# Kernel tuning notes

Measured on AMD Instinct MI355X. Metric: run time of the kernel, lower is better.

Reference implementation:

```python
import jax, jax.numpy as jnp
import numpy as np

B, N, T, L = 32, 716, 168, 64
SED, TED = 32, 4
TN_LAYERS, GCN_LAYERS = 2, 2
TCN_C = 16


def _gru_scan(xseq, Wih, Whh, bih, bhh):
    # torch nn.GRU (batch_first) math; xseq: (B,T,Din) -> (B,T,H)
    Bq = xseq.shape[0]
    H = Whh.shape[1]
    xw = xseq @ Wih.T + bih  # (B,T,3H)

    def step(h, xw_t):
        gh = h @ Whh.T + bhh
        xr, xz, xn = jnp.split(xw_t, 3, axis=-1)
        hr, hz, hn = jnp.split(gh, 3, axis=-1)
        r = jax.nn.sigmoid(xr + hr)
        z = jax.nn.sigmoid(xz + hz)
        n = jnp.tanh(xn + r * hn)
        h_new = (1.0 - z) * n + z * h
        return h_new, h_new

    h0 = jnp.zeros((Bq, H), xseq.dtype)
    _, hs = jax.lax.scan(step, h0, jnp.swapaxes(xw, 0, 1))
    return jnp.swapaxes(hs, 0, 1)


def setup_inputs() -> dict:
    key = jax.random.key(0)
    ks = jax.random.split(key, 20)
    r = lambda k, shp, s: jax.random.normal(k, shp, dtype=jnp.float32) * s
    z = lambda shp: jnp.zeros(shp, jnp.float32)
    din = T + SED
    gin = N + SED + TED
    inp = {
        'x': r(ks[0], (B, N, T), 1.0),
        'x_enc_mark': r(ks[1], (B, T, TED), 1.0),
        'se_emb': r(ks[2], (N, SED), 0.02),
        'se_W1': r(ks[3], (din, L), din ** -0.5), 'se_b1': z((L,)),
        'se_W2': r(ks[4], (L, L), L ** -0.5), 'se_b2': z((L,)),
        'te_emb': r(ks[5], (T, SED), 0.02),
        'te_Wih': r(ks[6], (3 * L, gin), gin ** -0.5),
        'te_Whh': r(ks[7], (3 * L, L), L ** -0.5),
        'te_bih': z((3 * L,)), 'te_bhh': z((3 * L,)),
        'gcn_W': r(ks[8], (TN_LAYERS, GCN_LAYERS, L, L), L ** -0.5),
        'gcn_b': z((TN_LAYERS, GCN_LAYERS, L)),
        'fr_W1': r(ks[9], (L, T), L ** -0.5), 'fr_b1': z((T,)),
        'fr_W2': r(ks[10], (T, T), T ** -0.5), 'fr_b2': z((T,)),
        'tr_Wih': r(ks[11], (3 * N, L), L ** -0.5),
        'tr_Whh': r(ks[12], (3 * N, N), N ** -0.5),
        'tr_bih': z((3 * N,)), 'tr_bhh': z((3 * N,)),
        'tcn_W0': r(ks[13], (TCN_C, 3, 1, 2), (3 * 2) ** -0.5), 'tcn_b0': z((TCN_C,)),
        'tcn_W1': r(ks[14], (TCN_C, TCN_C, 1, 2), (TCN_C * 2) ** -0.5), 'tcn_b1': z((TCN_C,)),
        'tcn_W2': r(ks[15], (TCN_C, TCN_C, 1, 2), (TCN_C * 2) ** -0.5), 'tcn_b2': z((TCN_C,)),
        'out_W': r(ks[16], (1, TCN_C, 1, 1), TCN_C ** -0.5), 'out_b': z((1,)),
    }
    return inp


def reference(x, x_enc_mark, se_emb, se_W1, se_b1, se_W2, se_b2,
              te_emb, te_Wih, te_Whh, te_bih, te_bhh,
              gcn_W, gcn_b, fr_W1, fr_b1, fr_W2, fr_b2,
              tr_Wih, tr_Whh, tr_bih, tr_bhh,
              tcn_W0, tcn_b0, tcn_W1, tcn_b1, tcn_W2, tcn_b2, out_W, out_b):
    Bq, Nq, Tq = x.shape
    elu = jax.nn.elu
    # ---- SpatialEncoder: (B,N,T) -> (B,N,L)
    se_in = jnp.concatenate([x, jnp.broadcast_to(se_emb, (Bq,) + se_emb.shape)], axis=2)
    Xs = elu(se_in @ se_W1 + se_b1) @ se_W2 + se_b2
    # ---- TemporalEncoder: GRU over (B,T,N+SED+TED) -> (B,T,L)
    te_in = jnp.concatenate([jnp.swapaxes(x, 1, 2), x_enc_mark,
                             jnp.broadcast_to(te_emb, (Bq,) + te_emb.shape)], axis=2)
    Xt = _gru_scan(te_in, te_Wih, te_Whh, te_bih, te_bhh)
    X = jnp.concatenate([Xs, Xt], axis=1)  # (B, N+T, L)
    # ---- TN modules: adaptive graph construction + message passing.
    # adj = tanh(relu(X X^T) + I). The torch code extracts nonzero edges per batch
    # and scatters messages over them; since zero weights contribute nothing,
    # edge-list message passing == dense weighted-adjacency matmul (vectorized here).
    eye = jnp.eye(Nq + Tq, dtype=x.dtype)
    for i in range(gcn_W.shape[0]):
        adj = jnp.tanh(jax.nn.relu(jnp.einsum('bnf,bmf->bnm', X, X)) + eye)
        h = X
        for j in range(gcn_W.shape[1]):
            h = elu(jnp.einsum('bnm,bmf->bnf', adj, h) @ gcn_W[i, j] + gcn_b[i, j])
        X = h
    Xs, Xt = X[:, :Nq, :], X[:, Nq:, :]
    # ---- rebuild heads
    n_out = elu(Xs @ fr_W1 + fr_b1) @ fr_W2 + fr_b2  # (B,N,T)
    t_out = _gru_scan(Xt, tr_Wih, tr_Whh, tr_bih, tr_bhh)  # (B,T,N)
    stacked = jnp.stack([n_out, jnp.swapaxes(t_out, 1, 2), x], axis=1)  # (B,3,N,T)
    # ---- TCN output layer: causal dilated convs along time, then 1x1 projection
    dn = ('NCHW', 'OIHW', 'NCHW')
    h = stacked
    for W, b, d in ((tcn_W0, tcn_b0, 1), (tcn_W1, tcn_b1, 2), (tcn_W2, tcn_b2, 4)):
        h = jax.lax.conv_general_dilated(h, W, (1, 1), ((0, 0), (d, 0)),
                                         rhs_dilation=(1, d), dimension_numbers=dn)
        h = elu(h + b[None, :, None, None])
    out = jax.lax.conv_general_dilated(h, out_W, (1, 1), 'VALID',
                                       dimension_numbers=dn) + out_b[None, :, None, None]
    return out[:, :, :, -1]  # (B, 1, N): one-step forecast per node
```

## Files before the change

kernel.cpp:

```cpp
#include <hip/hip_runtime.h>

#define B_   32
#define N_   716
#define T_   168
#define L_   64
#define NT_  884
#define NTP  896
#define TE3_ 192
#define TRH_ 716
#define TR3_ 2148
#define TR3P 2176
#define WSTR 744
#define HSTR 720
#define TRBLKS 90

typedef unsigned short u16;
typedef unsigned long long u64;
typedef __attribute__((ext_vector_type(8))) short short8;
typedef __attribute__((ext_vector_type(4))) float f32x4;

static __device__ __forceinline__ float eluf(float x){ return x > 0.f ? x : expm1f(x); }
static __device__ __forceinline__ float sigf(float x){ return 1.f/(1.f+expf(-x)); }
static __device__ __forceinline__ u16 f2bf(float f){
  unsigned u = __float_as_uint(f);
// ... 19 lines not shown
__global__ __launch_bounds__(256) void k_wihbf(const float* __restrict__ Wih, u16* __restrict__ WihB){
  int idx = blockIdx.x*256 + threadIdx.x;
  if (idx >= TR3P*L_) return;
  int r = idx >> 6;
  WihB[idx] = (r < TR3_) ? f2bf(Wih[idx]) : (u16)0;
}
__global__ __launch_bounds__(256) void k_wtb(const float* __restrict__ W,
                                             u16* __restrict__ WTh, u16* __restrict__ WTl){
  int l = blockIdx.x;
  for (int e = threadIdx.x; e < 4096; e += 256){
    int g = e >> 6, f = e & 63;
    float v = W[(size_t)l*4096 + f*64 + g];
    u16 hi = f2bf(v);
    WTh[(size_t)l*4096 + e] = hi;
    WTl[(size_t)l*4096 + e] = f2bf(v - bf2f(hi));
  }
}
__global__ __launch_bounds__(256) void k_sew(const float* __restrict__ W1, const float* __restrict__ W2,
    u16* __restrict__ w1h, u16* __restrict__ w1l, u16* __restrict__ w2h, u16* __restrict__ w2l){
  int tid = threadIdx.x;
  for (int e = tid; e < 64*224; e += 256){
    int g = e / 224, k = e % 224;
    float v = (k < 200) ? W1[k*64 + g] : 0.f;
    u16 hi = f2bf(v); w1h[e] = hi; w1l[e] = f2bf(v - bf2f(hi));
  }
  for (int e = tid; e < 4096; e += 256){
    int g = e >> 6, f = e & 63;
    float v = W2[f*64 + g];
    u16 hi = f2bf(v); w2h[e] = hi; w2l[e] = f2bf(v - bf2f(hi));
  }
}
__global__ __launch_bounds__(256) void k_frw(const float* __restrict__ W1, const float* __restrict__ W2,
    u16* __restrict__ w1h, u16* __restrict__ w1l, u16* __restrict__ w2h, u16* __restrict__ w2l){
  int tid = threadIdx.x;
  for (int e = tid; e < 176*64; e += 256){
    int n = e >> 6, k = e & 63;
    float v = (n < 168) ? W1[k*168 + n] : 0.f;
    u16 hi = f2bf(v); w1h[e] = hi; w1l[e] = f2bf(v - bf2f(hi));
  }
  for (int e = tid; e < 16*192; e += 256){
    int c = e / 192, k = e % 192;
    float v = (c < 8 && k < 168) ? W2[k*168 + 160 + c] : 0.f;
    u16 hi = f2bf(v); w2h[e] = hi; w2l[e] = f2bf(v - bf2f(hi));
  }
}
__global__ __launch_bounds__(256) void k_wte(const float* __restrict__ W, u16* __restrict__ wh, u16* __restrict__ wl){
  int idx = blockIdx.x*256 + threadIdx.x;
  if (idx >= 192*768) return;
  int g = idx / 768, k = idx % 768;
  float v = (k < 752) ? W[(size_t)g*752 + k] : 0.f;
  u16 hi = f2bf(v); wh[idx] = hi; wl[idx] = f2bf(v - bf2f(hi));
}

__global__ __launch_bounds__(256) void k_seinB(const float* __restrict__ x, const float* __restrict__ se_emb,
                                               u16* __restrict__ seh, u16* __restrict__ sel){
  int idx = blockIdx.x*256 + threadIdx.x;
  if (idx >= 22912*224) return;
  int k = idx % 224; int m = idx / 224;
  int b = m / N_, n = m - b*N_;
  float v = 0.f;
  if (k < 168) v = x[((size_t)b*N_ + n)*T_ + k];
  else if (k < 200) v = se_emb[n*32 + (k - 168)];
  u16 hi = f2bf(v);
  seh[idx] = hi; sel[idx] = f2bf(v - bf2f(hi));
}

__global__ __launch_bounds__(256) void k_sem(const u16* __restrict__ seh, const u16* __restrict__ sel,
    const u16* __restrict__ w1h, const u16* __restrict__ w1l,
    const u16* __restrict__ w2h, const u16* __restrict__ w2l,
    const float* __restrict__ b1, const float* __restrict__ b2, float* __restrict__ X){
  __shared__ u16 Tlh[64*72], Tll[64*72];
  int m0 = blockIdx.x*64;
  int tid = threadIdx.x, wv = tid >> 6, lane = tid & 63;
  const u16* Ah = seh + (size_t)(m0 + 16*wv + (lane & 15))*224 + (lane >> 4)*8;
  const u16* Al = sel + (size_t)(m0 + 16*wv + (lane & 15))*224 + (lane >> 4)*8;
  const u16* Bh = w1h + (lane & 15)*224 + (lane >> 4)*8;
  const u16* Bl = w1l + (lane & 15)*224 + (lane >> 4)*8;
  f32x4 hh[4], hl[4], lh[4];
  #pragma unroll
  for (int q = 0; q < 4; ++q){ hh[q]=(f32x4){0,0,0,0}; hl[q]=(f32x4){0,0,0,0}; lh[q]=(f32x4){0,0,0,0}; }
  #pragma unroll
  for (int kt = 0; kt < 7; ++kt){
    short8 ah = *(const short8*)(Ah + kt*32);
    short8 al = *(const short8*)(Al + kt*32);
    #pragma unroll
    for (int q = 0; q < 4; ++q){
      short8 bh = *(const short8*)(Bh + q*16*224 + kt*32);
      short8 bl = *(const short8*)(Bl + q*16*224 + kt*32);
      hh[q] = bmfma(ah, bh, hh[q]);
      hl[q] = bmfma(ah, bl, hl[q]);
      lh[q] = bmfma(al, bh, lh[q]);
    }
  }
  int mrow = 16*wv + (lane >> 4)*4;
  #pragma unroll
  for (int q = 0; q < 4; ++q){
    int g = q*16 + (lane & 15);
    float bv = b1[g];
    #pragma unroll
    for (int r = 0; r < 4; ++r){
      float v = eluf(hh[q][r] + hl[q][r] + lh[q][r] + bv);
      u16 hi = f2bf(v);
      Tlh[(mrow + r)*72 + g] = hi;
      Tll[(mrow + r)*72 + g] = f2bf(v - bf2f(hi));
    }
  }
  __syncthreads();
  const u16* A2h = Tlh + (16*wv + (lane & 15))*72 + (lane >> 4)*8;
  const u16* A2l = Tll + (16*wv + (lane & 15))*72 + (lane >> 4)*8;
  const u16* B2h = w2h + (lane & 15)*64 + (lane >> 4)*8;
  const u16* B2l = w2l + (lane & 15)*64 + (lane >> 4)*8;
  f32x4 ohh[4], ohl[4], olh[4];
  #pragma unroll
  for (int q = 0; q < 4; ++q){ ohh[q]=(f32x4){0,0,0,0}; ohl[q]=(f32x4){0,0,0,0}; olh[q]=(f32x4){0,0,0,0}; }
  #pragma unroll
  for (int kt = 0; kt < 2; ++kt){
    short8 a2h = *(const short8*)(A2h + kt*32);
    short8 a2l = *(const short8*)(A2l + kt*32);
    #pragma unroll
    for (int q = 0; q < 4; ++q){
      short8 b2h = *(const short8*)(B2h + q*16*64 + kt*32);
      short8 b2l = *(const short8*)(B2l + q*16*64 + kt*32);
      ohh[q] = bmfma(a2h, b2h, ohh[q]);
      ohl[q] = bmfma(a2h, b2l, ohl[q]);
      olh[q] = bmfma(a2l, b2h, olh[q]);
    }
  }
  #pragma unroll
// ... 39 lines not shown
  else if (c < 36) v = te_emb[t*32 + (c - 4)];
  u16 hi = f2bf(v);
  size_t o = (size_t)row*768 + 716 + c;
  th_[o] = hi; tl_[o] = f2bf(v - bf2f(hi));
}

__global__ __launch_bounds__(256) void k_texw(const u16* __restrict__ teh, const u16* __restrict__ tel,
    const u16* __restrict__ wh, const u16* __restrict__ wl,
    const float* __restrict__ bih, float* __restrict__ xwte){
  int m0 = blockIdx.x*64, n0 = blockIdx.y*64;
  int tid = threadIdx.x, wv = tid >> 6, lane = tid & 63;
  const u16* Ah = teh + (size_t)(m0 + 16*wv + (lane & 15))*768 + (lane >> 4)*8;
  const u16* Al = tel + (size_t)(m0 + 16*wv + (lane & 15))*768 + (lane >> 4)*8;
  const u16* Bh = wh + (size_t)(n0 + (lane & 15))*768 + (lane >> 4)*8;
  const u16* Bl = wl + (size_t)(n0 + (lane & 15))*768 + (lane >> 4)*8;
  f32x4 hh[4], hl[4], lh[4];
  #pragma unroll
  for (int q = 0; q < 4; ++q){ hh[q]=(f32x4){0,0,0,0}; hl[q]=(f32x4){0,0,0,0}; lh[q]=(f32x4){0,0,0,0}; }
  #pragma unroll 4
  for (int kt = 0; kt < 24; ++kt){
    short8 ah = *(const short8*)(Ah + kt*32);
    short8 al = *(const short8*)(Al + kt*32);
    #pragma unroll
    for (int q = 0; q < 4; ++q){
      short8 bh = *(const short8*)(Bh + q*16*768 + kt*32);
      short8 bl = *(const short8*)(Bl + q*16*768 + kt*32);
      hh[q] = bmfma(ah, bh, hh[q]);
      hl[q] = bmfma(ah, bl, hl[q]);
      lh[q] = bmfma(al, bh, lh[q]);
    }
  }
  int mb = m0 + 16*wv + (lane >> 4)*4;
  #pragma unroll
  for (int q = 0; q < 4; ++q){
    int g = n0 + q*16 + (lane & 15);
    float bv = bih[g];
    #pragma unroll
    for (int r = 0; r < 4; ++r)
      xwte[(size_t)(mb + r)*TE3_ + g] = hh[q][r] + hl[q][r] + lh[q][r] + bv;
  }
}

__global__ __launch_bounds__(192) void k_te_scan(const float* __restrict__ xw, const float* __restrict__ Whh,
                 const float* __restrict__ bhh, float* __restrict__ X){
  int b = blockIdx.x; int tid = threadIdx.x;
  __shared__ float Wsh[TE3_*65];
  __shared__ float hs[64];
  __shared__ float gh[TE3_];
  for (int l = tid; l < TE3_*64; l += 192){ int j = l >> 6, f = l & 63; Wsh[j*65+f] = Whh[l]; }
  if (tid < 64) hs[tid] = 0.f;
  __syncthreads();
  for (int t = 0; t < T_; ++t){
    const float* xr = xw + ((size_t)b*T_ + t)*TE3_;
    float g = bhh[tid];
    #pragma unroll 8
    for (int f = 0; f < 64; ++f) g = fmaf(hs[f], Wsh[tid*65+f], g);
    gh[tid] = g;
    __syncthreads();
    if (tid < 64){
      float r = sigf(xr[tid] + gh[tid]);
      float z = sigf(xr[64+tid] + gh[64+tid]);
      float n = tanhf(xr[128+tid] + r*gh[128+tid]);
      float hn = (1.f - z)*n + z*hs[tid];
      hs[tid] = hn;
      X[((size_t)b*NT_ + N_ + t)*L_ + tid] = hn;
    }
    __syncthreads();
  }
}

__global__ __launch_bounds__(256) void k_xbf(const float* __restrict__ X,
                 u16* __restrict__ Xbh, u16* __restrict__ Xbl,
                 u16* __restrict__ XTh, u16* __restrict__ XTl){
  __shared__ u16 th[32][33], tl[32][33];
  int b = blockIdx.z, i0 = blockIdx.x*32, f0 = blockIdx.y*32;
  int tx = threadIdx.x & 31, ty = threadIdx.x >> 5;
  for (int rr = ty; rr < 32; rr += 8){
    int i = i0 + rr, f = f0 + tx;
    float v = (i < NT_) ? X[((size_t)b*NT_ + i)*L_ + f] : 0.f;
    u16 hi = f2bf(v);
    u16 lo = f2bf(v - bf2f(hi));
    th[rr][tx] = hi; tl[rr][tx] = lo;
    Xbh[((size_t)b*NTP + i)*L_ + f] = hi;
    Xbl[((size_t)b*NTP + i)*L_ + f] = lo;
  }
  __syncthreads();
  for (int rr = ty; rr < 32; rr += 8){
    XTh[((size_t)b*L_ + f0 + rr)*NTP + i0 + tx] = th[tx][rr];
    XTl[((size_t)b*L_ + f0 + rr)*NTP + i0 + tx] = tl[tx][rr];
  }
}

__global__ __launch_bounds__(256) void k_adjb(const u16* __restrict__ Xbh, const u16* __restrict__ Xbl,
                                              u16* __restrict__ adjh, u16* __restrict__ adjl){
  int b = blockIdx.z, i0 = blockIdx.x*64, j0 = blockIdx.y*64;
  int tid = threadIdx.x, wv = tid >> 6, lane = tid & 63;
  const u16* Ah = Xbh + ((size_t)b*NTP + i0 + 16*wv + (lane & 15))*L_ + (lane >> 4)*8;
  const u16* Al = Xbl + ((size_t)b*NTP + i0 + 16*wv + (lane & 15))*L_ + (lane >> 4)*8;
  const u16* Bh = Xbh + ((size_t)b*NTP + j0 + (lane & 15))*L_ + (lane >> 4)*8;
  const u16* Bl = Xbl + ((size_t)b*NTP + j0 + (lane & 15))*L_ + (lane >> 4)*8;
  f32x4 chh[4], chl[4], clh[4];
  #pragma unroll
  for (int q = 0; q < 4; ++q){ chh[q] = (f32x4){0,0,0,0}; chl[q] = (f32x4){0,0,0,0}; clh[q] = (f32x4){0,0,0,0}; }
  #pragma unroll
  for (int kt = 0; kt < 2; ++kt){
    short8 ah = *(const short8*)(Ah + kt*32);
    short8 al = *(const short8*)(Al + kt*32);
    #pragma unroll
    for (int q = 0; q < 4; ++q){
      short8 bh = *(const short8*)(Bh + q*16*L_ + kt*32);
      short8 bl = *(const short8*)(Bl + q*16*L_ + kt*32);
      chh[q] = bmfma(ah, bh, chh[q]);
      chl[q] = bmfma(ah, bl, chl[q]);
      clh[q] = bmfma(al, bh, clh[q]);
    }
  }
  int ib = i0 + 16*wv + (lane >> 4)*4;
  int jb = j0 + (lane & 15);
  #pragma unroll
  for (int q = 0; q < 4; ++q){
    int j = jb + q*16;
    #pragma unroll
    for (int r = 0; r < 4; ++r){
      int i = ib + r;
      size_t idx = ((size_t)b*NTP + i)*NTP + j;
      if (i < NT_ && j < NT_){
        float v = tanhf(fmaxf(chh[q][r] + chl[q][r] + clh[q][r], 0.f) + (i == j ? 1.f : 0.f));
        u16 hi = f2bf(v);
        adjh[idx] = hi;
        adjl[idx] = f2bf(v - bf2f(hi));
      } else {
        adjh[idx] = 0; adjl[idx] = 0;
      }
    }
  }
}

__global__ __launch_bounds__(256) void k_gcnm(const u16* __restrict__ adjh, const u16* __restrict__ adjl,
                 const u16* __restrict__ hTh, const u16* __restrict__ hTl,
                 const u16* __restrict__ WTh, const u16* __restrict__ WTl,
                 const float* __restrict__ bias,
                 float* __restrict__ Y, u16* __restrict__ YTh, u16* __restrict__ YTl){
  __shared__ u16 Tlh[64*72], Tll[64*72];
  int b = blockIdx.y, i0 = blockIdx.x*64;
  int tid = threadIdx.x, wv = tid >> 6, lane = tid & 63;
  const u16* Ah = adjh + ((size_t)b*NTP + i0 + 16*wv + (lane & 15))*NTP + (lane >> 4)*8;
  const u16* Al = adjl + ((size_t)b*NTP + i0 + 16*wv + (lane & 15))*NTP + (lane >> 4)*8;
  const u16* Bh = hTh + ((size_t)b*L_ + (lane & 15))*NTP + (lane >> 4)*8;
  const u16* Bl = hTl + ((size_t)b*L_ + (lane & 15))*NTP + (lane >> 4)*8;
  f32x4 thh[4], thl[4], tlh[4];
  #pragma unroll
  for (int q = 0; q < 4; ++q){ thh[q] = (f32x4){0,0,0,0}; thl[q] = (f32x4){0,0,0,0}; tlh[q] = (f32x4){0,0,0,0}; }
  #pragma unroll 2
  for (int kt = 0; kt < 28; ++kt){
    short8 ah = *(const short8*)(Ah + kt*32);
    short8 al = *(const short8*)(Al + kt*32);
    #pragma unroll
    for (int q = 0; q < 4; ++q){
      short8 bh = *(const short8*)(Bh + q*16*NTP + kt*32);
      short8 bl = *(const short8*)(Bl + q*16*NTP + kt*32);
      thh[q] = bmfma(ah, bh, thh[q]);
      thl[q] = bmfma(ah, bl, thl[q]);
      tlh[q] = bmfma(al, bh, tlh[q]);
    }
  }
  {
    int mrow = 16*wv + (lane >> 4)*4;
    #pragma unroll
    for (int q = 0; q < 4; ++q)
      #pragma unroll
      for (int r = 0; r < 4; ++r){
        float v = thh[q][r] + thl[q][r] + tlh[q][r];
        u16 hi = f2bf(v);
        Tlh[(mrow + r)*72 + q*16 + (lane & 15)] = hi;
        Tll[(mrow + r)*72 + q*16 + (lane & 15)] = f2bf(v - bf2f(hi));
      }
  }
  __syncthreads();
  const u16* A2h = Tlh + (16*wv + (lane & 15))*72 + (lane >> 4)*8;
  const u16* A2l = Tll + (16*wv + (lane & 15))*72 + (lane >> 4)*8;
  const u16* B2h = WTh + (lane & 15)*L_ + (lane >> 4)*8;
  const u16* B2l = WTl + (lane & 15)*L_ + (lane >> 4)*8;
  f32x4 ohh[4], ohl[4], olh[4];
  #pragma unroll
  for (int q = 0; q < 4; ++q){ ohh[q] = (f32x4){0,0,0,0}; ohl[q] = (f32x4){0,0,0,0}; olh[q] = (f32x4){0,0,0,0}; }
  #pragma unroll
  for (int kt = 0; kt < 2; ++kt){
    short8 a2h = *(const short8*)(A2h + kt*32);
    short8 a2l = *(const short8*)(A2l + kt*32);
    #pragma unroll
    for (int q = 0; q < 4; ++q){
      short8 b2h = *(const short8*)(B2h + q*16*L_ + kt*32);
      short8 b2l = *(const short8*)(B2l + q*16*L_ + kt*32);
      ohh[q] = bmfma(a2h, b2h, ohh[q]);
      ohl[q] = bmfma(a2h, b2l, ohl[q]);
      olh[q] = bmfma(a2l, b2h, olh[q]);
    }
  }
  __syncthreads();
  {
    int mrow = 16*wv + (lane >> 4)*4;
    #pragma unroll
    for (int q = 0; q < 4; ++q){
      int g = q*16 + (lane & 15);
      float bv = bias[g];
      #pragma unroll
      for (int r = 0; r < 4; ++r){
        int i = i0 + mrow + r;
        float v = eluf(ohh[q][r] + ohl[q][r] + olh[q][r] + bv);
        if (i < NT_ && Y) Y[((size_t)b*NT_ + i)*L_ + g] = v;
        u16 hi = 0, lo = 0;
        if (i < NT_){ hi = f2bf(v); lo = f2bf(v - bf2f(hi)); }
        Tlh[g*72 + mrow + r] = hi;
        Tll[g*72 + mrow + r] = lo;
      }
    }
  }
  __syncthreads();
  {
    int g = tid >> 2, c = tid & 3;
    uint4* dh = (uint4*)(YTh + ((size_t)b*L_ + g)*NTP + i0 + c*16);
    uint4* dl = (uint4*)(YTl + ((size_t)b*L_ + g)*NTP + i0 + c*16);
    const uint4* sh = (const uint4*)(Tlh + g*72 + c*16);
    const uint4* sl = (const uint4*)(Tll + g*72 + c*16);
    dh[0] = sh[0]; dh[1] = sh[1];
    dl[0] = sl[0]; dl[1] = sl[1];
  }
}

__global__ __launch_bounds__(256) void k_frm(const u16* __restrict__ Xbh, const u16* __restrict__ Xbl,
    const u16* __restrict__ w1h, const u16* __restrict__ w1l,
    const u16* __restrict__ w2h, const u16* __restrict__ w2l,
    const float* __restrict__ b1, const float* __restrict__ b2, float* __restrict__ nout8){
  __shared__ u16 T1h[64*192], T1l[64*192];
  __shared__ u16 B2hl[16*192], B2ll[16*192];
  int m0 = blockIdx.x*64;
  int tid = threadIdx.x, wv = tid >> 6, lane = tid & 63;
  for (int o = tid; o < 768; o += 256){
    ((u64*)B2hl)[o] = ((const u64*)w2h)[o];
    ((u64*)B2ll)[o] = ((const u64*)w2l)[o];
  }
  for (int o = tid; o < 1024; o += 256){
    int rr = o >> 4, cc = o & 15;
    T1h[rr*192 + 176 + cc] = 0; T1l[rr*192 + 176 + cc] = 0;
  }
  int ar = m0 + 16*wv + (lane & 15);
  int ab = ar / N_, an = ar - ab*N_;
  const u16* Ah = Xbh + ((size_t)ab*NTP + an)*L_ + (lane >> 4)*8;
  const u16* Al = Xbl + ((size_t)ab*NTP + an)*L_ + (lane >> 4)*8;
  int mrow = 16*wv + (lane >> 4)*4;
  for (int tile = 0; tile < 11; ++tile){
    const u16* Bh = w1h + (tile*16 + (lane & 15))*64 + (lane >> 4)*8;
    const u16* Bl = w1l + (tile*16 + (lane & 15))*64 + (lane >> 4)*8;
    f32x4 shh={0,0,0,0}, shl={0,0,0,0}, slh={0,0,0,0};
    #pragma unroll
    for (int kt = 0; kt < 2; ++kt){
      short8 ah = *(const short8*)(Ah + kt*32);
      short8 al = *(const short8*)(Al + kt*32);
      short8 bh = *(const short8*)(Bh + kt*32);
      short8 bl = *(const short8*)(Bl + kt*32);
      shh = bmfma(ah, bh, shh);
      shl = bmfma(ah, bl, shl);
      slh = bmfma(al, bh, slh);
    }
    int col = tile*16 + (lane & 15);
    float bb = (col < 168) ? b1[col] : 0.f;
    #pragma unroll
    for (int r = 0; r < 4; ++r){
// ... 31 lines not shown
}

__global__ __launch_bounds__(256) void k_xtbufb(const float* __restrict__ X, u16* __restrict__ XtB){
  int idx = blockIdx.x*256 + threadIdx.x;
  if (idx >= T_*B_*L_) return;
  int f = idx & 63; int tb = idx >> 6; int bb = tb & 31; int t = tb >> 5;
  XtB[idx] = f2bf(X[((size_t)bb*NT_ + N_ + t)*L_ + f]);
}

__global__ __launch_bounds__(256) void k_xwm(const u16* __restrict__ XtB, const u16* __restrict__ WihB,
                                             const float* __restrict__ bih, float* __restrict__ xw){
  int m0 = blockIdx.x*64, n0 = blockIdx.y*64;
  int tid = threadIdx.x, wv = tid >> 6, lane = tid & 63;
  const u16* Ab = XtB + (size_t)(m0 + 16*wv + (lane & 15))*L_ + (lane >> 4)*8;
  const u16* Bb = WihB + (size_t)(n0 + (lane & 15))*L_ + (lane >> 4)*8;
  f32x4 c0={0,0,0,0}, c1={0,0,0,0}, c2={0,0,0,0}, c3={0,0,0,0};
  #pragma unroll
  for (int kt = 0; kt < 2; ++kt){
    short8 a = *(const short8*)(Ab + kt*32);
    c0 = bmfma(a, *(const short8*)(Bb + kt*32), c0);
    c1 = bmfma(a, *(const short8*)(Bb + 16*L_ + kt*32), c1);
    c2 = bmfma(a, *(const short8*)(Bb + 32*L_ + kt*32), c2);
    c3 = bmfma(a, *(const short8*)(Bb + 48*L_ + kt*32), c3);
  }
  int mb = m0 + 16*wv + (lane >> 4)*4;
  int nb = n0 + (lane & 15);
  f32x4 cc[4] = {c0, c1, c2, c3};
  #pragma unroll
  for (int q = 0; q < 4; ++q){
    int n = nb + q*16;
    if (n >= TR3_) continue;
    float bv = bih[n];
    #pragma unroll
    for (int r = 0; r < 4; ++r)
      xw[(size_t)(mb + r)*TR3_ + n] = cc[q][r] + bv;
  }
}

__global__ __launch_bounds__(192) void k_tr_scan(
    const u16* __restrict__ WhhB,
    const float* __restrict__ bhh,
    const float* __restrict__ xw,
    u16* __restrict__ hb0, u16* __restrict__ hb1,
    float* __restrict__ tout8,
    int* __restrict__ flags){
  __shared__ u16 w_lds[48*WSTR];
  __shared__ u16 h_lds[16*WSTR];
  __shared__ float g_lds[2*256];
  __shared__ float xw_lds[2][16*48];
  const int tid = threadIdx.x;
  const int wv = tid >> 6, lane = tid & 63;
  const int cb = blockIdx.x >> 1, hhalf = blockIdx.x & 1;
  const int k0 = cb*16, b0 = hhalf*16;

  {
    int row = tid / 12, c = tid % 12;
    int g = c >> 2, koff = (c & 3)*4;
    *(f32x4*)(&xw_lds[0][row*48 + g*16 + koff]) =
      *(const f32x4*)(xw + (size_t)(b0 + row)*TR3_ + g*TRH_ + k0 + koff);
  }
  for (int o = tid; o < 16*24; o += 192){
    int n = o / 24, c = o - n*24;
    h_lds[n*WSTR + 720 + c] = 0;
  }
  for (int r = 0; r < 48; ++r){
    int g = r >> 4, m = r & 15, k = k0 + m;
    bool kv = (k < TRH_);
    const uint2* src = (const uint2*)(WhhB + (size_t)(g*TRH_ + (kv ? k : 0))*TRH_);
    uint2* dst = (uint2*)(w_lds + r*WSTR);
    uint2 zz; zz.x = 0; zz.y = 0;
    for (int o = tid; o < 186; o += 192)
      dst[o] = (kv && o < 179) ? src[o] : zz;
  }
  const u16* arow = w_lds + (size_t)(wv*16 + (lane & 15))*WSTR + (lane >> 4)*8;
  const u16* brow = h_lds + (size_t)(lane & 15)*WSTR + (lane >> 4)*8;

  const int mb = (lane >> 4)*4;
  const int kx = k0 + mb;
  const bool kval = (kx < TRH_);
  const int bx = b0 + (lane & 15);
  f32x4 hp = {0.f, 0.f, 0.f, 0.f};
  f32x4 br4 = {0,0,0,0}, bz4 = {0,0,0,0}, bn4 = {0,0,0,0};
  if (wv == 0){
    int kc = kval ? kx : 0;
    br4 = *(const f32x4*)(bhh + kc);
    bz4 = *(const f32x4*)(bhh + TRH_ + kc);
    bn4 = *(const f32x4*)(bhh + 2*TRH_ + kc);
  }
  const int sn = tid / 12, sj = tid % 12;
  u16* const ldst = h_lds + sn*WSTR + sj*8;
  __syncthreads();

  for (int t = 0; t < T_; ++t){
    const u16* hcur = (t & 1) ? hb1 : hb0;
    u16* hnxt = (t & 1) ? hb0 : hb1;
    if (tid < 45){
      const int* fp = flags + (tid*2 + hhalf)*16;
      while (__hip_atomic_load(fp, __ATOMIC_RELAXED, __HIP_MEMORY_SCOPE_AGENT) < t){}
    }
    __syncthreads();
    {
      const u64* srow = (const u64*)(hcur + (size_t)(b0 + sn)*HSTR) + sj;
      u64 v0  = __hip_atomic_load(srow +   0, __ATOMIC_RELAXED, __HIP_MEMORY_SCOPE_AGENT);
      u64 v1  = __hip_atomic_load(srow +  12, __ATOMIC_RELAXED, __HIP_MEMORY_SCOPE_AGENT);
      u64 v2  = __hip_atomic_load(srow +  24, __ATOMIC_RELAXED, __HIP_MEMORY_SCOPE_AGENT);
      u64 v3  = __hip_atomic_load(srow +  36, __ATOMIC_RELAXED, __HIP_MEMORY_SCOPE_AGENT);
      u64 v4  = __hip_atomic_load(srow +  48, __ATOMIC_RELAXED, __HIP_MEMORY_SCOPE_AGENT);
      u64 v5  = __hip_atomic_load(srow +  60, __ATOMIC_RELAXED, __HIP_MEMORY_SCOPE_AGENT);
      u64 v6  = __hip_atomic_load(srow +  72, __ATOMIC_RELAXED, __HIP_MEMORY_SCOPE_AGENT);
      u64 v7  = __hip_atomic_load(srow +  84, __ATOMIC_RELAXED, __HIP_MEMORY_SCOPE_AGENT);
      u64 v8  = __hip_atomic_load(srow +  96, __ATOMIC_RELAXED, __HIP_MEMORY_SCOPE_AGENT);
      u64 v9  = __hip_atomic_load(srow + 108, __ATOMIC_RELAXED, __HIP_MEMORY_SCOPE_AGENT);
      u64 v10 = __hip_atomic_load(srow + 120, __ATOMIC_RELAXED, __HIP_MEMORY_SCOPE_AGENT);
      u64 v11 = __hip_atomic_load(srow + 132, __ATOMIC_RELAXED, __HIP_MEMORY_SCOPE_AGENT);
      u64 v12 = __hip_atomic_load(srow + 144, __ATOMIC_RELAXED, __HIP_MEMORY_SCOPE_AGENT);
      u64 v13 = __hip_atomic_load(srow + 156, __ATOMIC_RELAXED, __HIP_MEMORY_SCOPE_AGENT);
      u64 v14 = __hip_atomic_load(srow + 168, __ATOMIC_RELAXED, __HIP_MEMORY_SCOPE_AGENT);
      u64* d = (u64*)(h_lds + sn*WSTR) + sj;
      d[0]      = v0;   d[12]     = v1;   d[24]     = v2;   d[36]     = v3;
      d[48]     = v4;   d[60]     = v5;   d[72]     = v6;   d[84]     = v7;
      d[96]     = v8;   d[108]    = v9;   d[120]    = v10;  d[132]    = v11;
      d[144]    = v12;  d[156]    = v13;  d[168]    = v14;
    }
    __syncthreads();
    f32x4 a0={0,0,0,0}, a1={0,0,0,0}, a2={0,0,0,0}, a3={0,0,0,0};
    for (int kt = 0; kt < 20; kt += 4){
      a0 = bmfma(*(const short8*)(arow + kt*32),     *(const short8*)(brow + kt*32),     a0);
      a1 = bmfma(*(const short8*)(arow + (kt+1)*32), *(const short8*)(brow + (kt+1)*32), a1);
      a2 = bmfma(*(const short8*)(arow + (kt+2)*32), *(const short8*)(brow + (kt+2)*32), a2);
      a3 = bmfma(*(const short8*)(arow + (kt+3)*32), *(const short8*)(brow + (kt+3)*32), a3);
    }
    a0 = bmfma(*(const short8*)(arow + 20*32), *(const short8*)(brow + 20*32), a0);
    a1 = bmfma(*(const short8*)(arow + 21*32), *(const short8*)(brow + 21*32), a1);
    a2 = bmfma(*(const short8*)(arow + 22*32), *(const short8*)(brow + 22*32), a2);
    f32x4 acc = (a0 + a1) + (a2 + a3);
    if (wv){
      #pragma unroll
      for (int r = 0; r < 4; ++r) g_lds[(wv-1)*256 + lane*4 + r] = acc[r];
    }
    __syncthreads();
    if (wv == 0 && kval){
      const float* xb = &xw_lds[t & 1][(lane & 15)*48];
      float hnew[4];
      #pragma unroll
      for (int r = 0; r < 4; ++r){
        float rg = sigf(xb[mb + r] + acc[r] + br4[r]);
        float zg = sigf(xb[16 + mb + r] + g_lds[lane*4 + r] + bz4[r]);
        float ng = tanhf(xb[32 + mb + r] + rg*(g_lds[256 + lane*4 + r] + bn4[r]));
        hnew[r] = (1.f - zg)*ng + zg*hp[r];
        hp[r] = hnew[r];
      }
      u64 pk = (u64)((unsigned)f2bf(hnew[0]) | ((unsigned)f2bf(hnew[1]) << 16))
             | ((u64)((unsigned)f2bf(hnew[2]) | ((unsigned)f2bf(hnew[3]) << 16)) << 32);
      __hip_atomic_store((u64*)(hnxt + (size_t)bx*HSTR + kx), pk,
                         __ATOMIC_RELAXED, __HIP_MEMORY_SCOPE_AGENT);
      if (t >= 160){
        #pragma unroll
        for (int r = 0; r < 4; ++r)
          tout8[(size_t)(bx*TRH_ + kx + r)*8 + (t - 160)] = hnew[r];
      }
    }
    if (wv == 0){
      asm volatile("s_waitcnt vmcnt(0)" ::: "memory");
      if (lane == 0)
        __hip_atomic_store(flags + blockIdx.x*16, t + 1,
                           __ATOMIC_RELAXED, __HIP_MEMORY_SCOPE_AGENT);
    }
    if (t + 1 < T_){
      int row = tid / 12, c = tid % 12;
      int g = c >> 2, koff = (c & 3)*4;
      *(f32x4*)(&xw_lds[(t + 1) & 1][row*48 + g*16 + koff]) =
        *(const f32x4*)(xw + (size_t)((t+1)*32 + b0 + row)*TR3_ + g*TRH_ + k0 + koff);
    }
  }
  (void)ldst;
}

__global__ __launch_bounds__(256) void k_tcn(const float* __restrict__ nout8, const float* __restrict__ tout8,
                 const float* __restrict__ x,
                 const float* __restrict__ W0, const float* __restrict__ b0,
                 const float* __restrict__ W1, const float* __restrict__ b1,
                 const float* __restrict__ W2, const float* __restrict__ b2,
                 const float* __restrict__ oW, const float* __restrict__ ob,
                 float* __restrict__ out){
  __shared__ float w0s[96], b0s[16], w1s[512], b1s[16], w2s[512], b2s[16], ows[16], obs;
  int tid = threadIdx.x;
  for (int l = tid; l < 96; l += 256) w0s[l] = W0[l];
  for (int l = tid; l < 512; l += 256){ w1s[l] = W1[l]; w2s[l] = W2[l]; }
  if (tid < 16){ b0s[tid]=b0[tid]; b1s[tid]=b1[tid]; b2s[tid]=b2[tid]; ows[tid]=oW[tid]; }
  if (tid == 0) obs = ob[0];
  __syncthreads();
  int idx = blockIdx.x*256 + tid;
  if (idx >= B_*N_) return;
  int b = idx / N_, n = idx % N_;
  float s0[8], s1[8], s2[8];
  #pragma unroll
  for (int i = 0; i < 8; ++i){
    s0[i] = nout8[(size_t)idx*8 + i];
    s1[i] = tout8[(size_t)idx*8 + i];
    s2[i] = x[((size_t)b*N_ + n)*T_ + 160 + i];
  }
  float h1[16][4];
  #pragma unroll
  for (int c = 0; c < 16; ++c)
    #pragma unroll
    for (int q = 0; q < 4; ++q){
      int tt = 2*q + 1;
      float v = b0s[c]
        + w0s[c*6+0]*s0[tt-1] + w0s[c*6+1]*s0[tt]
        + w0s[c*6+2]*s1[tt-1] + w0s[c*6+3]*s1[tt]
        + w0s[c*6+4]*s2[tt-1] + w0s[c*6+5]*s2[tt];
      h1[c][q] = eluf(v);
    }
  float h2[16][2];
  #pragma unroll
  for (int c = 0; c < 16; ++c){
    float v3 = b1s[c], v7 = b1s[c];
    #pragma unroll
    for (int i2 = 0; i2 < 16; ++i2){
      v3 += w1s[c*32+i2*2]*h1[i2][0] + w1s[c*32+i2*2+1]*h1[i2][1];
      v7 += w1s[c*32+i2*2]*h1[i2][2] + w1s[c*32+i2*2+1]*h1[i2][3];
    }
    h2[c][0] = eluf(v3); h2[c][1] = eluf(v7);
  }
  float o = obs;
  #pragma unroll
  for (int c = 0; c < 16; ++c){
    float v = b2s[c];
// ... 27 lines not shown
  const float* fr_W2   = (const float*)d_in[16];
  const float* fr_b2   = (const float*)d_in[17];
  const float* tr_Wih  = (const float*)d_in[18];
  const float* tr_Whh  = (const float*)d_in[19];
  const float* tr_bih  = (const float*)d_in[20];
  const float* tr_bhh  = (const float*)d_in[21];
  const float* tcn_W0  = (const float*)d_in[22];
  const float* tcn_b0  = (const float*)d_in[23];
  const float* tcn_W1  = (const float*)d_in[24];
  const float* tcn_b1  = (const float*)d_in[25];
  const float* tcn_W2  = (const float*)d_in[26];
  const float* tcn_b2  = (const float*)d_in[27];
  const float* out_W   = (const float*)d_in[28];
  const float* out_b   = (const float*)d_in[29];
  float* out = (float*)d_out;
  (void)in_sizes; (void)n_in; (void)out_size; (void)ws_size;

  char* ws = (char*)d_ws;
  size_t off = 0;
  auto alloc = [&](size_t bytes)->void*{
    void* p = (void*)(ws + off); off += (bytes + 255) & ~(size_t)255; return p; };
  float* X       = (float*)alloc((size_t)B_*NT_*L_*4);
  u16*   adjh    = (u16*)  alloc((size_t)B_*NTP*NTP*2);
  u16*   adjl    = (u16*)  alloc((size_t)B_*NTP*NTP*2);
  u16*   XtB     = (u16*)  alloc((size_t)T_*B_*L_*2);
  u16*   WihB    = (u16*)  alloc((size_t)TR3P*L_*2);
  u16*   WhhB    = (u16*)  alloc((size_t)TR3_*TRH_*2);
  u16*   Xbh     = (u16*)  alloc((size_t)B_*NTP*L_*2);
  u16*   Xbl     = (u16*)  alloc((size_t)B_*NTP*L_*2);
  u16*   hTah    = (u16*)  alloc((size_t)B_*L_*NTP*2);
  u16*   hTal    = (u16*)  alloc((size_t)B_*L_*NTP*2);
  u16*   hTbh    = (u16*)  alloc((size_t)B_*L_*NTP*2);
  u16*   hTbl    = (u16*)  alloc((size_t)B_*L_*NTP*2);
  u16*   WTh     = (u16*)  alloc((size_t)4*4096*2);
  u16*   WTl     = (u16*)  alloc((size_t)4*4096*2);
  u16*   w1seh   = (u16*)  alloc((size_t)64*224*2);
  u16*   w1sel   = (u16*)  alloc((size_t)64*224*2);
  u16*   w2seh   = (u16*)  alloc((size_t)4096*2);
  u16*   w2sel   = (u16*)  alloc((size_t)4096*2);
  u16*   w1frh   = (u16*)  alloc((size_t)176*64*2);
  u16*   w1frl   = (u16*)  alloc((size_t)176*64*2);
  u16*   w2frh   = (u16*)  alloc((size_t)16*192*2);
  u16*   w2frl   = (u16*)  alloc((size_t)16*192*2);
  u16*   wteh    = (u16*)  alloc((size_t)192*768*2);
  u16*   wtel    = (u16*)  alloc((size_t)192*768*2);
  u16*   hb0     = (u16*)  alloc((size_t)B_*HSTR*2);
  u16*   hb1     = (u16*)  alloc((size_t)B_*HSTR*2);
  int*   flags   = (int*)  alloc(8192);
  float* nout8   = (float*)alloc((size_t)B_*N_*8*4);
  float* tout8   = (float*)alloc((size_t)B_*N_*8*4);
  u16*   teinh   = (u16*)adjh;
  u16*   teinl   = (u16*)((char*)adjh +  8257536);
  float* te_xw   = (float*)((char*)adjh + 16515072);
  u16*   seh     = (u16*)((char*)adjh + 20643840);
  u16*   sel     = (u16*)((char*)adjh + 30908416);
  float* xw      = (float*)adjl;

  hipMemsetAsync(hb0, 0, (size_t)B_*HSTR*2*2 + 8192, stream);

  k_whhbf<<<(TR3_*TRH_/4 + 255)/256, 256, 0, stream>>>(tr_Whh, WhhB, TR3_*TRH_/4);
  k_wihbf<<<(TR3P*L_ + 255)/256, 256, 0, stream>>>(tr_Wih, WihB);
  k_wtb<<<4, 256, 0, stream>>>(gcn_W, WTh, WTl);
  k_sew<<<1, 256, 0, stream>>>(se_W1, se_W2, w1seh, w1sel, w2seh, w2sel);
  k_frw<<<1, 256, 0, stream>>>(fr_W1, fr_W2, w1frh, w1frl, w2frh, w2frl);
  k_wte<<<(192*768 + 255)/256, 256, 0, stream>>>(te_Wih, wteh, wtel);
  k_seinB<<<(22912*224 + 255)/256, 256, 0, stream>>>(x, se_emb, seh, sel);
  k_sem<<<358, 256, 0, stream>>>(seh, sel, w1seh, w1sel, w2seh, w2sel, se_b1, se_b2, X);
  k_teinx_b<<<dim3(23,6,B_), 256, 0, stream>>>(x, teinh, teinl);
  k_teinr_b<<<(B_*T_*52 + 255)/256, 256, 0, stream>>>(mark, te_emb, teinh, teinl);
  k_texw<<<dim3(84,3), 256, 0, stream>>>(teinh, teinl, wteh, wtel, te_bih, te_xw);
  k_te_scan<<<B_, 192, 0, stream>>>(te_xw, te_Whh, te_bhh, X);
  for (int i = 0; i < 2; ++i){
    k_xbf<<<dim3(28,2,B_),256,0,stream>>>(X, Xbh, Xbl, hTah, hTal);
    k_adjb<<<dim3(14,14,B_),256,0,stream>>>(Xbh, Xbl, adjh, adjl);
    k_gcnm<<<dim3(14,B_),256,0,stream>>>(adjh, adjl, hTah, hTal,
        WTh + (i*2+0)*4096, WTl + (i*2+0)*4096, gcn_b + (i*2+0)*64, nullptr, hTbh, hTbl);
    k_gcnm<<<dim3(14,B_),256,0,stream>>>(adjh, adjl, hTbh, hTbl,
        WTh + (i*2+1)*4096, WTl + (i*2+1)*4096, gcn_b + (i*2+1)*64, X, hTah, hTal);
  }
  k_xbf<<<dim3(28,2,B_),256,0,stream>>>(X, Xbh, Xbl, hTah, hTal);
  k_frm<<<358, 256, 0, stream>>>(Xbh, Xbl, w1frh, w1frl, w2frh, w2frl, fr_b1, fr_b2, nout8);
  k_xtbufb<<<(T_*B_*L_+255)/256,256,0,stream>>>(X, XtB);
  k_xwm<<<dim3(84,34),256,0,stream>>>(XtB, WihB, tr_bih, xw);
  k_tr_scan<<<TRBLKS,192,0,stream>>>(WhhB, tr_bhh, xw, hb0, hb1, tout8, flags);
  k_tcn<<<(B_*N_+255)/256,256,0,stream>>>(nout8, tout8, x,
      tcn_W0, tcn_b0, tcn_W1, tcn_b1, tcn_W2, tcn_b2, out_W, out_b, out);
}
```

Measured before the change: 1.447 ms.

## Fuse adjacency build into GCN matmul, fuse SE input conversion, prefetch scan inputs

Replaces the separate adjacency kernel plus the GCN kernel with one fused kernel. Each 64-row block recomputes 64x64 adjacency tiles from X in shared memory and consumes them right away, so the full bf16 hi/lo adjacency matrices are never written to or read from global memory. The adjacency is now recomputed in both GCN layers, so the X·X^T work is done twice per iteration. Separately, the SE input split/convert is moved into the SE matmul kernel via shared memory, the TE scan dot product gets four independent accumulators, the final xbf call skips its unused transpose, and the TR scan issues its next-step xw load before the MFMA loop.

```diff
diff --git a/kernel.cpp b/kernel.cpp
--- a/kernel.cpp
+++ b/kernel.cpp
@@ -95,28 +95,26 @@
   u16 hi = f2bf(v); wh[idx] = hi; wl[idx] = f2bf(v - bf2f(hi));
 }
 
-__global__ __launch_bounds__(256) void k_seinB(const float* __restrict__ x, const float* __restrict__ se_emb,
-                                               u16* __restrict__ seh, u16* __restrict__ sel){
-  int idx = blockIdx.x*256 + threadIdx.x;
-  if (idx >= 22912*224) return;
-  int k = idx % 224; int m = idx / 224;
-  int b = m / N_, n = m - b*N_;
-  float v = 0.f;
-  if (k < 168) v = x[((size_t)b*N_ + n)*T_ + k];
-  else if (k < 200) v = se_emb[n*32 + (k - 168)];
-  u16 hi = f2bf(v);
-  seh[idx] = hi; sel[idx] = f2bf(v - bf2f(hi));
-}
-
-__global__ __launch_bounds__(256) void k_sem(const u16* __restrict__ seh, const u16* __restrict__ sel,
+__global__ __launch_bounds__(256) void k_sem(const float* __restrict__ x, const float* __restrict__ se_emb,
     const u16* __restrict__ w1h, const u16* __restrict__ w1l,
     const u16* __restrict__ w2h, const u16* __restrict__ w2l,
     const float* __restrict__ b1, const float* __restrict__ b2, float* __restrict__ X){
+  __shared__ u16 Sh[64*232], Sl[64*232];
   __shared__ u16 Tlh[64*72], Tll[64*72];
   int m0 = blockIdx.x*64;
   int tid = threadIdx.x, wv = tid >> 6, lane = tid & 63;
-  const u16* Ah = seh + (size_t)(m0 + 16*wv + (lane & 15))*224 + (lane >> 4)*8;
-  const u16* Al = sel + (size_t)(m0 + 16*wv + (lane & 15))*224 + (lane >> 4)*8;
+  for (int o = tid; o < 64*224; o += 256){
+    int r = o / 224, k = o - (o/224)*224;
+    int m = m0 + r; int b = m / N_, n = m - b*N_;
+    float v = 0.f;
+    if (k < 168) v = x[((size_t)b*N_ + n)*T_ + k];
+    else if (k < 200) v = se_emb[n*32 + (k - 168)];
+    u16 hi = f2bf(v);
+    Sh[r*232 + k] = hi; Sl[r*232 + k] = f2bf(v - bf2f(hi));
+  }
+  __syncthreads();
+  const u16* Ah = Sh + (16*wv + (lane & 15))*232 + (lane >> 4)*8;
+  const u16* Al = Sl + (16*wv + (lane & 15))*232 + (lane >> 4)*8;
   const u16* Bh = w1h + (lane & 15)*224 + (lane >> 4)*8;
   const u16* Bl = w1l + (lane & 15)*224 + (lane >> 4)*8;
   f32x4 hh[4], hl[4], lh[4];
@@ -262,10 +260,15 @@
   __syncthreads();
   for (int t = 0; t < T_; ++t){
     const float* xr = xw + ((size_t)b*T_ + t)*TE3_;
-    float g = bhh[tid];
-    #pragma unroll 8
-    for (int f = 0; f < 64; ++f) g = fmaf(hs[f], Wsh[tid*65+f], g);
-    gh[tid] = g;
+    float g0 = bhh[tid], g1 = 0.f, g2 = 0.f, g3 = 0.f;
+    #pragma unroll
+    for (int f = 0; f < 64; f += 4){
+      g0 = fmaf(hs[f],   Wsh[tid*65+f],   g0);
+      g1 = fmaf(hs[f+1], Wsh[tid*65+f+1], g1);
+      g2 = fmaf(hs[f+2], Wsh[tid*65+f+2], g2);
+      g3 = fmaf(hs[f+3], Wsh[tid*65+f+3], g3);
+    }
+    gh[tid] = (g0 + g1) + (g2 + g3);
     __syncthreads();
     if (tid < 64){
       float r = sigf(xr[tid] + gh[tid]);
@@ -294,6 +297,7 @@
     Xbh[((size_t)b*NTP + i)*L_ + f] = hi;
     Xbl[((size_t)b*NTP + i)*L_ + f] = lo;
   }
+  if (!XTh) return;
   __syncthreads();
   for (int rr = ty; rr < 32; rr += 8){
     XTh[((size_t)b*L_ + f0 + rr)*NTP + i0 + tx] = th[tx][rr];
@@ -301,91 +305,92 @@
   }
 }
 
-__global__ __launch_bounds__(256) void k_adjb(const u16* __restrict__ Xbh, const u16* __restrict__ Xbl,
-                                              u16* __restrict__ adjh, u16* __restrict__ adjl){
-  int b = blockIdx.z, i0 = blockIdx.x*64, j0 = blockIdx.y*64;
-  int tid = threadIdx.x, wv = tid >> 6, lane = tid & 63;
-  const u16* Ah = Xbh + ((size_t)b*NTP + i0 + 16*wv + (lane & 15))*L_ + (lane >> 4)*8;
-  const u16* Al = Xbl + ((size_t)b*NTP + i0 + 16*wv + (lane & 15))*L_ + (lane >> 4)*8;
-  const u16* Bh = Xbh + ((size_t)b*NTP + j0 + (lane & 15))*L_ + (lane >> 4)*8;
-  const u16* Bl = Xbl + ((size_t)b*NTP + j0 + (lane & 15))*L_ + (lane >> 4)*8;
-  f32x4 chh[4], chl[4], clh[4];
-  #pragma unroll
-  for (int q = 0; q < 4; ++q){ chh[q] = (f32x4){0,0,0,0}; chl[q] = (f32x4){0,0,0,0}; clh[q] = (f32x4){0,0,0,0}; }
-  #pragma unroll
-  for (int kt = 0; kt < 2; ++kt){
-    short8 ah = *(const short8*)(Ah + kt*32);
-    short8 al = *(const short8*)(Al + kt*32);
-    #pragma unroll
-    for (int q = 0; q < 4; ++q){
-      short8 bh = *(const short8*)(Bh + q*16*L_ + kt*32);
-      short8 bl = *(const short8*)(Bl + q*16*L_ + kt*32);
-      chh[q] = bmfma(ah, bh, chh[q]);
-      chl[q] = bmfma(ah, bl, chl[q]);
-      clh[q] = bmfma(al, bh, clh[q]);
-    }
-  }
-  int ib = i0 + 16*wv + (lane >> 4)*4;
-  int jb = j0 + (lane & 15);
-  #pragma unroll
-  for (int q = 0; q < 4; ++q){
-    int j = jb + q*16;
-    #pragma unroll
-    for (int r = 0; r < 4; ++r){
-      int i = ib + r;
-      size_t idx = ((size_t)b*NTP + i)*NTP + j;
-      if (i < NT_ && j < NT_){
-        float v = tanhf(fmaxf(chh[q][r] + chl[q][r] + clh[q][r], 0.f) + (i == j ? 1.f : 0.f));
-        u16 hi = f2bf(v);
-        adjh[idx] = hi;
-        adjl[idx] = f2bf(v - bf2f(hi));
-      } else {
-        adjh[idx] = 0; adjl[idx] = 0;
-      }
-    }
-  }
-}
-
-__global__ __launch_bounds__(256) void k_gcnm(const u16* __restrict__ adjh, const u16* __restrict__ adjl,
-                 const u16* __restrict__ hTh, const u16* __restrict__ hTl,
-                 const u16* __restrict__ WTh, const u16* __restrict__ WTl,
-                 const float* __restrict__ bias,
-                 float* __restrict__ Y, u16* __restrict__ YTh, u16* __restrict__ YTl){
+__global__ __launch_bounds__(256) void k_gcnf(
+    const u16* __restrict__ Xbh, const u16* __restrict__ Xbl,
+    const u16* __restrict__ hTh, const u16* __restrict__ hTl,
+    const u16* __restrict__ WTh, const u16* __restrict__ WTl,
+    const float* __restrict__ bias,
+    float* __restrict__ Y, u16* __restrict__ YTh, u16* __restrict__ YTl){
+  __shared__ u16 AJh[64*72], AJl[64*72];
   __shared__ u16 Tlh[64*72], Tll[64*72];
   int b = blockIdx.y, i0 = blockIdx.x*64;
   int tid = threadIdx.x, wv = tid >> 6, lane = tid & 63;
-  const u16* Ah = adjh + ((size_t)b*NTP + i0 + 16*wv + (lane & 15))*NTP + (lane >> 4)*8;
-  const u16* Al = adjl + ((size_t)b*NTP + i0 + 16*wv + (lane & 15))*NTP + (lane >> 4)*8;
-  const u16* Bh = hTh + ((size_t)b*L_ + (lane & 15))*NTP + (lane >> 4)*8;
-  const u16* Bl = hTl + ((size_t)b*L_ + (lane & 15))*NTP + (lane >> 4)*8;
+  const u16* XAh = Xbh + ((size_t)b*NTP + i0 + 16*wv + (lane & 15))*L_ + (lane >> 4)*8;
+  const u16* XAl = Xbl + ((size_t)b*NTP + i0 + 16*wv + (lane & 15))*L_ + (lane >> 4)*8;
+  const int ib = i0 + 16*wv + (lane >> 4)*4;
+  const int mrow = 16*wv + (lane >> 4)*4;
   f32x4 thh[4], thl[4], tlh[4];
   #pragma unroll
   for (int q = 0; q < 4; ++q){ thh[q] = (f32x4){0,0,0,0}; thl[q] = (f32x4){0,0,0,0}; tlh[q] = (f32x4){0,0,0,0}; }
-  #pragma unroll 2
-  for (int kt = 0; kt < 28; ++kt){
-    short8 ah = *(const short8*)(Ah + kt*32);
-    short8 al = *(const short8*)(Al + kt*32);
-    #pragma unroll
-    for (int q = 0; q < 4; ++q){
-      short8 bh = *(const short8*)(Bh + q*16*NTP + kt*32);
-      short8 bl = *(const short8*)(Bl + q*16*NTP + kt*32);
-      thh[q] = bmfma(ah, bh, thh[q]);
-      thl[q] = bmfma(ah, bl, thl[q]);
-      tlh[q] = bmfma(al, bh, tlh[q]);
-    }
-  }
-  {
-    int mrow = 16*wv + (lane >> 4)*4;
-    #pragma unroll
-    for (int q = 0; q < 4; ++q)
+  for (int jt = 0; jt < 14; ++jt){
+    int j0 = jt*64;
+    {
+      const u16* XBh = Xbh + ((size_t)b*NTP + j0 + (lane & 15))*L_ + (lane >> 4)*8;
+      const u16* XBl = Xbl + ((size_t)b*NTP + j0 + (lane & 15))*L_ + (lane >> 4)*8;
+      f32x4 chh[4], chl[4], clh[4];
       #pragma unroll
-      for (int r = 0; r < 4; ++r){
-        float v = thh[q][r] + thl[q][r] + tlh[q][r];
-        u16 hi = f2bf(v);
-        Tlh[(mrow + r)*72 + q*16 + (lane & 15)] = hi;
-        Tll[(mrow + r)*72 + q*16 + (lane & 15)] = f2bf(v - bf2f(hi));
+      for (int q = 0; q < 4; ++q){ chh[q] = (f32x4){0,0,0,0}; chl[q] = (f32x4){0,0,0,0}; clh[q] = (f32x4){0,0,0,0}; }
+      #pragma unroll
+      for (int kt = 0; kt < 2; ++kt){
+        short8 ah = *(const short8*)(XAh + kt*32);
+        short8 al = *(const short8*)(XAl + kt*32);
+        #pragma unroll
+        for (int q = 0; q < 4; ++q){
+          short8 bh = *(const short8*)(XBh + q*16*L_ + kt*32);
+          short8 bl = *(const short8*)(XBl + q*16*L_ + kt*32);
+          chh[q] = bmfma(ah, bh, chh[q]);
+          chl[q] = bmfma(ah, bl, chl[q]);
+          clh[q] = bmfma(al, bh, clh[q]);
+        }
       }
-  }
+      int jb = j0 + (lane & 15);
+      #pragma unroll
+      for (int q = 0; q < 4; ++q){
+        int j = jb + q*16;
+        #pragma unroll
+        for (int r = 0; r < 4; ++r){
+          int i = ib + r;
+          u16 hi = 0, lo = 0;
+          if (i < NT_ && j < NT_){
+            float v = tanhf(fmaxf(chh[q][r] + chl[q][r] + clh[q][r], 0.f) + (i == j ? 1.f : 0.f));
+            hi = f2bf(v); lo = f2bf(v - bf2f(hi));
+          }
+          AJh[(mrow + r)*72 + q*16 + (lane & 15)] = hi;
+          AJl[(mrow + r)*72 + q*16 + (lane & 15)] = lo;
+        }
+      }
+    }
+    __syncthreads();
+    {
+      const u16* A1h = AJh + (16*wv + (lane & 15))*72 + (lane >> 4)*8;
+      const u16* A1l = AJl + (16*wv + (lane & 15))*72 + (lane >> 4)*8;
+      const u16* B1h = hTh + ((size_t)b*L_ + (lane & 15))*NTP + j0 + (lane >> 4)*8;
+      const u16* B1l = hTl + ((size_t)b*L_ + (lane & 15))*NTP + j0 + (lane >> 4)*8;
+      #pragma unroll
+      for (int kt = 0; kt < 2; ++kt){
+        short8 ah = *(const short8*)(A1h + kt*32);
+        short8 al = *(const short8*)(A1l + kt*32);
+        #pragma unroll
+        for (int q = 0; q < 4; ++q){
+          short8 bh = *(const short8*)(B1h + q*16*NTP + kt*32);
+          short8 bl = *(const short8*)(B1l + q*16*NTP + kt*32);
+          thh[q] = bmfma(ah, bh, thh[q]);
+          thl[q] = bmfma(ah, bl, thl[q]);
+          tlh[q] = bmfma(al, bh, tlh[q]);
+        }
+      }
+    }
+    __syncthreads();
+  }
+  #pragma unroll
+  for (int q = 0; q < 4; ++q)
+    #pragma unroll
+    for (int r = 0; r < 4; ++r){
+      float v = thh[q][r] + thl[q][r] + tlh[q][r];
+      u16 hi = f2bf(v);
+      Tlh[(mrow + r)*72 + q*16 + (lane & 15)] = hi;
+      Tll[(mrow + r)*72 + q*16 + (lane & 15)] = f2bf(v - bf2f(hi));
+    }
   __syncthreads();
   const u16* A2h = Tlh + (16*wv + (lane & 15))*72 + (lane >> 4)*8;
   const u16* A2l = Tll + (16*wv + (lane & 15))*72 + (lane >> 4)*8;
@@ -408,22 +413,19 @@
     }
   }
   __syncthreads();
-  {
-    int mrow = 16*wv + (lane >> 4)*4;
-    #pragma unroll
-    for (int q = 0; q < 4; ++q){
-      int g = q*16 + (lane & 15);
-      float bv = bias[g];
-      #pragma unroll
-      for (int r = 0; r < 4; ++r){
-        int i = i0 + mrow + r;
-        float v = eluf(ohh[q][r] + ohl[q][r] + olh[q][r] + bv);
-        if (i < NT_ && Y) Y[((size_t)b*NT_ + i)*L_ + g] = v;
-        u16 hi = 0, lo = 0;
-        if (i < NT_){ hi = f2bf(v); lo = f2bf(v - bf2f(hi)); }
-        Tlh[g*72 + mrow + r] = hi;
-        Tll[g*72 + mrow + r] = lo;
-      }
+  #pragma unroll
+  for (int q = 0; q < 4; ++q){
+    int g = q*16 + (lane & 15);
+    float bv = bias[g];
+    #pragma unroll
+    for (int r = 0; r < 4; ++r){
+      int i = i0 + mrow + r;
+      float v = eluf(ohh[q][r] + ohl[q][r] + olh[q][r] + bv);
+      if (i < NT_ && Y) Y[((size_t)b*NT_ + i)*L_ + g] = v;
+      u16 hi = 0, lo = 0;
+      if (i < NT_){ hi = f2bf(v); lo = f2bf(v - bf2f(hi)); }
+      Tlh[g*72 + mrow + r] = hi;
+      Tll[g*72 + mrow + r] = lo;
     }
   }
   __syncthreads();
@@ -561,13 +563,11 @@
   const int wv = tid >> 6, lane = tid & 63;
   const int cb = blockIdx.x >> 1, hhalf = blockIdx.x & 1;
   const int k0 = cb*16, b0 = hhalf*16;
-
-  {
-    int row = tid / 12, c = tid % 12;
-    int g = c >> 2, koff = (c & 3)*4;
-    *(f32x4*)(&xw_lds[0][row*48 + g*16 + koff]) =
-      *(const f32x4*)(xw + (size_t)(b0 + row)*TR3_ + g*TRH_ + k0 + koff);
-  }
+  const int prow = tid / 12, pc = tid % 12;
+  const int pg = pc >> 2, pkoff = (pc & 3)*4;
+
+  *(f32x4*)(&xw_lds[0][prow*48 + pg*16 + pkoff]) =
+    *(const f32x4*)(xw + (size_t)(b0 + prow)*TR3_ + pg*TRH_ + k0 + pkoff);
   for (int o = tid; o < 16*24; o += 192){
     int n = o / 24, c = o - n*24;
     h_lds[n*WSTR + 720 + c] = 0;
@@ -597,7 +597,6 @@
     bn4 = *(const f32x4*)(bhh + 2*TRH_ + kc);
   }
   const int sn = tid / 12, sj = tid % 12;
-  u16* const ldst = h_lds + sn*WSTR + sj*8;
   __syncthreads();
 
   for (int t = 0; t < T_; ++t){
@@ -632,6 +631,10 @@
       d[144]    = v12;  d[156]    = v13;  d[168]    = v14;
     }
     __syncthreads();
+    f32x4 pf;
+    const bool haspf = (t + 1 < T_);
+    if (haspf)
+      pf = *(const f32x4*)(xw + (size_t)((t+1)*32 + b0 + prow)*TR3_ + pg*TRH_ + k0 + pkoff);
     f32x4 a0={0,0,0,0}, a1={0,0,0,0}, a2={0,0,0,0}, a3={0,0,0,0};
     for (int kt = 0; kt < 20; kt += 4){
       a0 = bmfma(*(const short8*)(arow + kt*32),     *(const short8*)(brow + kt*32),     a0);
@@ -675,14 +678,9 @@
         __hip_atomic_store(flags + blockIdx.x*16, t + 1,
                            __ATOMIC_RELAXED, __HIP_MEMORY_SCOPE_AGENT);
     }
-    if (t + 1 < T_){
-      int row = tid / 12, c = tid % 12;
-      int g = c >> 2, koff = (c & 3)*4;
-      *(f32x4*)(&xw_lds[(t + 1) & 1][row*48 + g*16 + koff]) =
-        *(const f32x4*)(xw + (size_t)((t+1)*32 + b0 + row)*TR3_ + g*TRH_ + k0 + koff);
-    }
-  }
-  (void)ldst;
+    if (haspf)
+      *(f32x4*)(&xw_lds[(t + 1) & 1][prow*48 + pg*16 + pkoff]) = pf;
+  }
 }
 
 __global__ __launch_bounds__(256) void k_tcn(const float* __restrict__ nout8, const float* __restrict__ tout8,
@@ -816,8 +814,6 @@
   u16*   teinh   = (u16*)adjh;
   u16*   teinl   = (u16*)((char*)adjh +  8257536);
   float* te_xw   = (float*)((char*)adjh + 16515072);
-  u16*   seh     = (u16*)((char*)adjh + 20643840);
-  u16*   sel     = (u16*)((char*)adjh + 30908416);
   float* xw      = (float*)adjl;
 
   hipMemsetAsync(hb0, 0, (size_t)B_*HSTR*2*2 + 8192, stream);
@@ -828,21 +824,19 @@
   k_sew<<<1, 256, 0, stream>>>(se_W1, se_W2, w1seh, w1sel, w2seh, w2sel);
   k_frw<<<1, 256, 0, stream>>>(fr_W1, fr_W2, w1frh, w1frl, w2frh, w2frl);
   k_wte<<<(192*768 + 255)/256, 256, 0, stream>>>(te_Wih, wteh, wtel);
-  k_seinB<<<(22912*224 + 255)/256, 256, 0, stream>>>(x, se_emb, seh, sel);
-  k_sem<<<358, 256, 0, stream>>>(seh, sel, w1seh, w1sel, w2seh, w2sel, se_b1, se_b2, X);
+  k_sem<<<358, 256, 0, stream>>>(x, se_emb, w1seh, w1sel, w2seh, w2sel, se_b1, se_b2, X);
   k_teinx_b<<<dim3(23,6,B_), 256, 0, stream>>>(x, teinh, teinl);
   k_teinr_b<<<(B_*T_*52 + 255)/256, 256, 0, stream>>>(mark, te_emb, teinh, teinl);
   k_texw<<<dim3(84,3), 256, 0, stream>>>(teinh, teinl, wteh, wtel, te_bih, te_xw);
   k_te_scan<<<B_, 192, 0, stream>>>(te_xw, te_Whh, te_bhh, X);
   for (int i = 0; i < 2; ++i){
     k_xbf<<<dim3(28,2,B_),256,0,stream>>>(X, Xbh, Xbl, hTah, hTal);
-    k_adjb<<<dim3(14,14,B_),256,0,stream>>>(Xbh, Xbl, adjh, adjl);
-    k_gcnm<<<dim3(14,B_),256,0,stream>>>(adjh, adjl, hTah, hTal,
+    k_gcnf<<<dim3(14,B_),256,0,stream>>>(Xbh, Xbl, hTah, hTal,
         WTh + (i*2+0)*4096, WTl + (i*2+0)*4096, gcn_b + (i*2+0)*64, nullptr, hTbh, hTbl);
-    k_gcnm<<<dim3(14,B_),256,0,stream>>>(adjh, adjl, hTbh, hTbl,
+    k_gcnf<<<dim3(14,B_),256,0,stream>>>(Xbh, Xbl, hTbh, hTbl,
         WTh + (i*2+1)*4096, WTl + (i*2+1)*4096, gcn_b + (i*2+1)*64, X, hTah, hTal);
   }
-  k_xbf<<<dim3(28,2,B_),256,0,stream>>>(X, Xbh, Xbl, hTah, hTal);
+  k_xbf<<<dim3(28,2,B_),256,0,stream>>>(X, Xbh, Xbl, nullptr, nullptr);
   k_frm<<<358, 256, 0, stream>>>(Xbh, Xbl, w1frh, w1frl, w2frh, w2frl, fr_b1, fr_b2, nout8);
   k_xtbufb<<<(T_*B_*L_+255)/256,256,0,stream>>>(X, XtB);
   k_xwm<<<dim3(84,34),256,0,stream>>>(XtB, WihB, tr_bih, xw);
```

Result: no change. 1.448 ms (+0.1%).
